# Optimization experiments

Measured on AMD Instinct MI355X. Metric: run time of the kernel, lower is better.

The kernel has to match this reference:

```python
import jax, jax.numpy as jnp
import numpy as np
import math

N_NODES = 100000
N_EDGES = 1600000
IN_FEATS = 128
H_FEATS = 64
NUM_CLASSES = 2
D = 2  # num_layers -> d+1 = 3 filters, each polynomial of degree d


def _calc_thetas(d):
    # Beta-Bernstein polynomial coefficients, ascending powers of x.
    # f_i(x) = (x/2)^i (1-x/2)^(d-i) / B(i+1, d+1-i),  B = i!(d-i)!/(d+1)!
    thetas = []
    for i in range(d + 1):
        beta = math.factorial(i) * math.factorial(d - i) / math.factorial(d + 1)
        p = np.array([1.0])
        for _ in range(i):
            p = np.convolve(p, [0.0, 0.5])
        for _ in range(d - i):
            p = np.convolve(p, [1.0, -0.5])
        thetas.append([float(c) for c in (p / beta)])
    return thetas

THETAS = _calc_thetas(D)


def setup_inputs() -> dict:
    key = jax.random.key(0)
    ks = jax.random.split(key, 12)
    x = jax.random.normal(ks[0], (N_NODES, IN_FEATS), dtype=jnp.float32)
    edge_index = jax.random.randint(ks[1], (2, N_EDGES), 0, N_NODES, dtype=jnp.int64)
    s = 0.05
    W1 = jax.random.normal(ks[2], (IN_FEATS, H_FEATS), jnp.float32) * s
    b1 = jnp.zeros((H_FEATS,), jnp.float32)
    W2 = jax.random.normal(ks[3], (H_FEATS, H_FEATS), jnp.float32) * s
    b2 = jnp.zeros((H_FEATS,), jnp.float32)
    Wm1 = jax.random.normal(ks[4], (H_FEATS * len(THETAS), H_FEATS), jnp.float32) * s
    bm1 = jnp.zeros((H_FEATS,), jnp.float32)
    Wm2 = jax.random.normal(ks[5], (H_FEATS, NUM_CLASSES), jnp.float32) * s
    bm2 = jnp.zeros((NUM_CLASSES,), jnp.float32)
    return {"x": x, "edge_index": edge_index, "W1": W1, "b1": b1,
            "W2": W2, "b2": b2, "Wm1": Wm1, "bm1": bm1, "Wm2": Wm2, "bm2": bm2}


def reference(x, edge_index, W1, b1, W2, b2, Wm1, bm1, Wm2, bm2):
    N = x.shape[0]
    src, dst = edge_index[0], edge_index[1]
    # in-degrees (edges point src -> dst, message summed at dst)
    deg = jax.ops.segment_sum(jnp.ones((edge_index.shape[1],), x.dtype), dst,
                              num_segments=N)
    dinv = jnp.clip(deg, 1.0, None) ** -0.5  # [N]
    dinv = dinv[:, None]
    # two linear + ReLU layers
    h = jax.nn.relu(x @ W1 + b1)
    h = jax.nn.relu(h @ W2 + b2)
    # PolyConv per theta: feat <- feat - D^-1/2 A D^-1/2 feat; acc += theta_k feat
    outs = []
    for theta in THETAS:
        feat = h
        acc = theta[0] * feat
        for k in range(1, len(theta)):
            msg = jax.ops.segment_sum((feat * dinv)[src], dst, num_segments=N)
            feat = feat - msg * dinv
            acc = acc + theta[k] * feat
        outs.append(acc)
    h_final = jnp.concatenate(outs, axis=-1)  # [N, h_feats*(d+1)]
    # MLP (2 layers): Linear -> ReLU -> Linear
    h_final = jax.nn.relu(h_final @ Wm1 + bm1)
    return h_final @ Wm2 + bm2
```

## Files before the change

### kernel.cpp

```cpp
#include <hip/hip_runtime.h>
#include <math.h>

#define N_NODES 100000
#define N_EDGES 1600000
#define IN_F 128
#define H_F 64

#define NBKT 196
#define BSEG 16384
#define BCAP 14336

#define NP        100096
#define OFF_CNT   0
#define OFF_MPK   256
#define OFF_W1H   6400
#define OFF_W1L   10496
#define OFF_W2H   14592
#define OFF_W2L   16640
#define OFF_OFFS  18688
#define OFF_D2    (OFF_OFFS + NP + 64)
#define OFF_RD    (OFF_D2 + NP)
#define OFF_DINV  (OFF_RD + NP)
#define OFF_ADJ   (OFF_DINV + NP)
#define OFF_H0    (OFF_ADJ + N_EDGES)
#define OFF_H1    (OFF_H0 + N_NODES*32)
#define OFF_H2    (OFF_H1 + N_NODES*32)

typedef __attribute__((ext_vector_type(8))) short bf16x8;
typedef __attribute__((ext_vector_type(4))) float f32x4;

__device__ __forceinline__ unsigned short bf16rn(float f) {
    unsigned u = __float_as_uint(f);
    u += 0x7FFFu + ((u >> 16) & 1u);
    return (unsigned short)(u >> 16);
}
#define UNPK(u, lo, hi) { lo = __uint_as_float((u) << 16); hi = __uint_as_float((u) & 0xFFFF0000u); }

__global__ __launch_bounds__(256) void k_prep(const float* __restrict__ Wm1,
        const float* __restrict__ W1, const float* __restrict__ W2,
        unsigned short* __restrict__ mpk,
        unsigned short* __restrict__ w1h, unsigned short* __restrict__ w1l,
        unsigned short* __restrict__ w2h, unsigned short* __restrict__ w2l) {
    int idx = blockIdx.x * 256 + threadIdx.x;
    if (idx < 12288) {
        int j = idx & 7;
        int n = (idx >> 3) & 63;
        int qd = (idx >> 9) & 3;
        int s = idx >> 11;
        int k = s * 32 + qd * 8 + j;
        int p = k >> 6;
        int kk = k & 63;
        float w0 = Wm1[kk * 64 + n];
        float w1 = Wm1[(64 + kk) * 64 + n];
        float w2 = Wm1[(128 + kk) * 64 + n];
        float v;
        if (p == 0)      v = 3.0f * w0;
        else if (p == 1) v = 3.0f * (w1 - w0);
        else             v = 0.75f * (w0 + w2) - 1.5f * w1;
        mpk[idx] = bf16rn(v);
    } else if (idx < 12288 + 8192) {
        int lin = idx - 12288;
        int j = lin & 7, cc = (lin >> 3) & 15, ot = (lin >> 7) & 3;
        int qd = (lin >> 9) & 3, ks = lin >> 11;
        float v = W1[(ks * 32 + qd * 8 + j) * 64 + ot * 16 + cc];
        unsigned short h = bf16rn(v);
        w1h[lin] = h;
        w1l[lin] = bf16rn(v - __uint_as_float((unsigned)h << 16));
    } else if (idx < 24576) {
        int lin = idx - 20480;
        int j = lin & 7, cc = (lin >> 3) & 15, ot = (lin >> 7) & 3;
        int qd = (lin >> 9) & 3, ks = lin >> 11;
        float v = W2[(ks * 32 + qd * 8 + j) * 64 + ot * 16 + cc];
        unsigned short h = bf16rn(v);
        w2h[lin] = h;
        w2l[lin] = bf16rn(v - __uint_as_float((unsigned)h << 16));
    }
}

__global__ __launch_bounds__(256) void k_bin(const int* __restrict__ src,
        const int* __restrict__ dst, int* __restrict__ cnt,
        int* __restrict__ binned, int E) {
    __shared__ int hist[4][208];
    __shared__ int cur4[4][208];
    int t = threadIdx.x;
    int w = t >> 6;
    for (int i = t; i < 4 * 208; i += 256) (&hist[0][0])[i] = 0;
    __syncthreads();
    int base = blockIdx.x * 4096 + t;
    int d[16];
    #pragma unroll
    for (int i = 0; i < 16; ++i) {
        int e = base + i * 256;
        int dd = (e < E) ? dst[e] : -1;
        d[i] = dd;
        if (dd >= 0) atomicAdd(&hist[w][dd >> 9], 1);
    }
    __syncthreads();
    if (t < NBKT) {
        int h0 = hist[0][t], h1 = hist[1][t], h2 = hist[2][t], h3 = hist[3][t];
        int tot = h0 + h1 + h2 + h3;
        int b0 = (tot > 0) ? atomicAdd(&cnt[t], tot) : 0;
        cur4[0][t] = b0;
        cur4[1][t] = b0 + h0;
        cur4[2][t] = b0 + h0 + h1;
        cur4[3][t] = b0 + h0 + h1 + h2;
    }
    __syncthreads();
    #pragma unroll
    for (int i = 0; i < 16; ++i) {
        int e = base + i * 256;
        if (e < E) {
            int s = src[e];
            int dd = d[i];
            int b = dd >> 9;
            int p = atomicAdd(&cur4[w][b], 1);
            if (p < BSEG) binned[b * BSEG + p] = ((dd & 511) << 17) | s;
        }
    }
}

__global__ __launch_bounds__(256) void k_cfill(const int* __restrict__ binned,
        const int* __restrict__ cnt, int* __restrict__ offs, int* __restrict__ adj,
        float* __restrict__ d2a, float* __restrict__ rda, float* __restrict__ dinva) {
    __shared__ int csum[256];
    __shared__ int degl[512];
    __shared__ int offl[512];
    __shared__ int curl[512];
    __shared__ int wsum[4];
    __shared__ int adjl[BCAP];
    int b = blockIdx.x, t = threadIdx.x;
    int cv = (t < NBKT) ? cnt[t] : 0;
    csum[t] = cv;
    __syncthreads();
    #pragma unroll
    for (int off = 1; off < 256; off <<= 1) {
        int u = (t >= off) ? csum[t - off] : 0;
        __syncthreads();
        csum[t] += u;
        __syncthreads();
    }
    int baseb = (b == 0) ? 0 : csum[b - 1];
    int cntb = csum[b] - baseb;
    if (b == 0 && t == 0) offs[N_NODES] = N_EDGES;
    int n0 = b << 9;
    const int* bp = binned + b * BSEG;
    degl[2 * t] = 0; degl[2 * t + 1] = 0;
    __syncthreads();
    for (int i = t; i < cntb; i += 256) {
        int w = bp[i];
        atomicAdd(&degl[w >> 17], 1);
    }
    __syncthreads();
    int d0 = degl[2 * t], d1 = degl[2 * t + 1];
    int tot = d0 + d1;
    int lane = t & 63, wid = t >> 6;
    int inc = tot;
    #pragma unroll
    for (int off = 1; off < 64; off <<= 1) {
        int v = __shfl_up(inc, off, 64);
        if (lane >= off) inc += v;
    }
    if (lane == 63) wsum[wid] = inc;
    __syncthreads();
    int wb = 0;
    for (int w = 0; w < wid; ++w) wb += wsum[w];
    int excl = wb + inc - tot;
    offl[2 * t] = excl;          curl[2 * t] = excl;
    offl[2 * t + 1] = excl + d0; curl[2 * t + 1] = excl + d0;
    __syncthreads();
    #pragma unroll
    for (int rep = 0; rep < 2; ++rep) {
        int i = t + rep * 256;
        int n = n0 + i;
        if (n < N_NODES) {
            offs[n] = baseb + offl[i];
            float df = (float)degl[i];
            if (df < 1.f) df = 1.f;
            float di = 1.0f / sqrtf(df);
            dinva[n] = di;
            d2a[n] = di * di;
            rda[n] = sqrtf(df);
        }
    }
    for (int i = t; i < cntb; i += 256) {
        int w = bp[i];
        int loc = w >> 17;
        int s = w & 0x1FFFF;
        int p = atomicAdd(&curl[loc], 1);
        if (p < BCAP) adjl[p] = s;
        else adj[baseb + p] = s;
    }
    __syncthreads();
    int lim = cntb < BCAP ? cntb : BCAP;
    for (int i = t; i < lim; i += 256) adj[baseb + i] = adjl[i];
}

__global__ __launch_bounds__(256) void k_gemm12(const float* __restrict__ x,
        const unsigned short* __restrict__ w1h, const unsigned short* __restrict__ w1l,
        const unsigned short* __restrict__ w2h, const unsigned short* __restrict__ w2l,
        const float* __restrict__ b1, const float* __restrict__ b2,
        const float* __restrict__ dinva, unsigned short* __restrict__ gsh, int N) {
    __shared__ unsigned int Hl[4][16 * 65];
    __shared__ unsigned short Sl[4][16 * 66];
    int t = threadIdx.x;
    int w = t >> 6, lane = t & 63;
    int c = lane & 15, qd = lane >> 4;
    int nbase = blockIdx.x * 64 + w * 16;
    if (nbase >= N) return;
    int node = nbase + c;
    int nclamp = (node < N) ? node : N - 1;

    f32x4 a0 = {0.f,0.f,0.f,0.f}, a1 = a0, a2 = a0, a3 = a0;
    #pragma unroll
    for (int ks = 0; ks < 4; ++ks) {
        const float* xp = x + (size_t)nclamp * IN_F + ks * 32 + qd * 8;
        float4 xa = *(const float4*)xp;
        float4 xb = *(const float4*)(xp + 4);
        float xs[8] = {xa.x, xa.y, xa.z, xa.w, xb.x, xb.y, xb.z, xb.w};
        bf16x8 ahi, alo;
        #pragma unroll
        for (int j = 0; j < 8; ++j) {
            unsigned short h = bf16rn(xs[j]);
            ahi[j] = (short)h;
            alo[j] = (short)bf16rn(xs[j] - __uint_as_float((unsigned)h << 16));
        }
        const unsigned short* bh = w1h + (size_t)(ks * 4 + qd) * 512;
        const unsigned short* bl = w1l + (size_t)(ks * 4 + qd) * 512;
        bf16x8 h0 = *(const bf16x8*)(bh + 0 * 128 + c * 8);
        bf16x8 l0 = *(const bf16x8*)(bl + 0 * 128 + c * 8);
        bf16x8 h1 = *(const bf16x8*)(bh + 1 * 128 + c * 8);
        bf16x8 l1 = *(const bf16x8*)(bl + 1 * 128 + c * 8);
        bf16x8 h2 = *(const bf16x8*)(bh + 2 * 128 + c * 8);
        bf16x8 l2 = *(const bf16x8*)(bl + 2 * 128 + c * 8);
        bf16x8 h3 = *(const bf16x8*)(bh + 3 * 128 + c * 8);
        bf16x8 l3 = *(const bf16x8*)(bl + 3 * 128 + c * 8);
        a0 = __builtin_amdgcn_mfma_f32_16x16x32_bf16(ahi, h0, a0, 0, 0, 0);
        a1 = __builtin_amdgcn_mfma_f32_16x16x32_bf16(ahi, h1, a1, 0, 0, 0);
        a2 = __builtin_amdgcn_mfma_f32_16x16x32_bf16(ahi, h2, a2, 0, 0, 0);
        a3 = __builtin_amdgcn_mfma_f32_16x16x32_bf16(ahi, h3, a3, 0, 0, 0);
        a0 = __builtin_amdgcn_mfma_f32_16x16x32_bf16(alo, h0, a0, 0, 0, 0);
        a1 = __builtin_amdgcn_mfma_f32_16x16x32_bf16(alo, h1, a1, 0, 0, 0);
        a2 = __builtin_amdgcn_mfma_f32_16x16x32_bf16(alo, h2, a2, 0, 0, 0);
        a3 = __builtin_amdgcn_mfma_f32_16x16x32_bf16(alo, h3, a3, 0, 0, 0);
        a0 = __builtin_amdgcn_mfma_f32_16x16x32_bf16(ahi, l0, a0, 0, 0, 0);
        a1 = __builtin_amdgcn_mfma_f32_16x16x32_bf16(ahi, l1, a1, 0, 0, 0);
        a2 = __builtin_amdgcn_mfma_f32_16x16x32_bf16(ahi, l2, a2, 0, 0, 0);
        a3 = __builtin_amdgcn_mfma_f32_16x16x32_bf16(ahi, l3, a3, 0, 0, 0);
    }
    #pragma unroll
    for (int ot = 0; ot < 4; ++ot) {
        float bb = b1[ot * 16 + c];
        f32x4 a = (ot == 0) ? a0 : (ot == 1) ? a1 : (ot == 2) ? a2 : a3;
        #pragma unroll
        for (int r = 0; r < 4; ++r) {
            float h = fmaxf(a[r] + bb, 0.f);
            unsigned short hh = bf16rn(h);
            unsigned short hl = bf16rn(h - __uint_as_float((unsigned)hh << 16));
            Hl[w][(qd * 4 + r) * 65 + ot * 16 + c] = ((unsigned)hh << 16) | hl;
        }
    }
    f32x4 d0 = {0.f,0.f,0.f,0.f}, d1 = d0, d2 = d0, d3 = d0;
    #pragma unroll
    for (int ks = 0; ks < 2; ++ks) {
        bf16x8 ahi, alo;
        #pragma unroll
        for (int j = 0; j < 8; ++j) {
            unsigned v = Hl[w][c * 65 + ks * 32 + qd * 8 + j];
            ahi[j] = (short)(v >> 16);
            alo[j] = (short)(v & 0xFFFFu);
        }
        const unsigned short* bh = w2h + (size_t)(ks * 4 + qd) * 512;
        const unsigned short* bl = w2l + (size_t)(ks * 4 + qd) * 512;
        bf16x8 h0 = *(const bf16x8*)(bh + 0 * 128 + c * 8);
        bf16x8 l0 = *(const bf16x8*)(bl + 0 * 128 + c * 8);
        bf16x8 h1 = *(const bf16x8*)(bh + 1 * 128 + c * 8);
        bf16x8 l1 = *(const bf16x8*)(bl + 1 * 128 + c * 8);
        bf16x8 h2 = *(const bf16x8*)(bh + 2 * 128 + c * 8);
        bf16x8 l2 = *(const bf16x8*)(bl + 2 * 128 + c * 8);
        bf16x8 h3 = *(const bf16x8*)(bh + 3 * 128 + c * 8);
        bf16x8 l3 = *(const bf16x8*)(bl + 3 * 128 + c * 8);
        d0 = __builtin_amdgcn_mfma_f32_16x16x32_bf16(ahi, h0, d0, 0, 0, 0);
        d1 = __builtin_amdgcn_mfma_f32_16x16x32_bf16(ahi, h1, d1, 0, 0, 0);
        d2 = __builtin_amdgcn_mfma_f32_16x16x32_bf16(ahi, h2, d2, 0, 0, 0);
        d3 = __builtin_amdgcn_mfma_f32_16x16x32_bf16(ahi, h3, d3, 0, 0, 0);
        d0 = __builtin_amdgcn_mfma_f32_16x16x32_bf16(alo, h0, d0, 0, 0, 0);
        d1 = __builtin_amdgcn_mfma_f32_16x16x32_bf16(alo, h1, d1, 0, 0, 0);
        d2 = __builtin_amdgcn_mfma_f32_16x16x32_bf16(alo, h2, d2, 0, 0, 0);
        d3 = __builtin_amdgcn_mfma_f32_16x16x32_bf16(alo, h3, d3, 0, 0, 0);
        d0 = __builtin_amdgcn_mfma_f32_16x16x32_bf16(ahi, l0, d0, 0, 0, 0);
        d1 = __builtin_amdgcn_mfma_f32_16x16x32_bf16(ahi, l1, d1, 0, 0, 0);
        d2 = __builtin_amdgcn_mfma_f32_16x16x32_bf16(ahi, l2, d2, 0, 0, 0);
        d3 = __builtin_amdgcn_mfma_f32_16x16x32_bf16(ahi, l3, d3, 0, 0, 0);
    }
    #pragma unroll
    for (int ot = 0; ot < 4; ++ot) {
        float bb = b2[ot * 16 + c];
        f32x4 a = (ot == 0) ? d0 : (ot == 1) ? d1 : (ot == 2) ? d2 : d3;
        #pragma unroll
        for (int r = 0; r < 4; ++r) {
            int nd = nbase + qd * 4 + r;
            float di = dinva[(nd < N) ? nd : N - 1];
            Sl[w][(qd * 4 + r) * 66 + ot * 16 + c] = bf16rn(di * fmaxf(a[r] + bb, 0.f));
        }
    }
    #pragma unroll
    for (int i = 0; i < 4; ++i) {
        int nl = i * 4 + qd;
        int nd = nbase + nl;
        if (nd < N) {
            ushort4 v;
            v.x = Sl[w][nl * 66 + c * 4 + 0];
            v.y = Sl[w][nl * 66 + c * 4 + 1];
            v.z = Sl[w][nl * 66 + c * 4 + 2];
            v.w = Sl[w][nl * 66 + c * 4 + 3];
            *(ushort4*)(gsh + (size_t)nd * 64 + c * 4) = v;
        }
    }
}

__global__ __launch_bounds__(256) void k_prop(const unsigned short* __restrict__ gh,
        unsigned short* __restrict__ gout, const int* __restrict__ offs,
        const int* __restrict__ adj, const float* __restrict__ d2a, int N) {
    int t = threadIdx.x;
    int lane = t & 63;
    int g = lane >> 3;
    int q = lane & 7;
    int n = blockIdx.x * 4 + (t >> 6);
    if (n >= N) return;
    int beg = offs[n], end = offs[n + 1];
    float a0 = 0.f, a1 = 0.f, a2 = 0.f, a3 = 0.f;
    float a4 = 0.f, a5 = 0.f, a6 = 0.f, a7 = 0.f;
    int e = beg + g;
    for (; e + 24 < end; e += 32) {
        int s0 = adj[e], s1 = adj[e + 8], s2 = adj[e + 16], s3 = adj[e + 24];
        uint4 v0 = *(const uint4*)(gh + (size_t)s0 * 64 + 8 * q);
        uint4 v1 = *(const uint4*)(gh + (size_t)s1 * 64 + 8 * q);
        uint4 v2 = *(const uint4*)(gh + (size_t)s2 * 64 + 8 * q);
        uint4 v3 = *(const uint4*)(gh + (size_t)s3 * 64 + 8 * q);
        float l, h;
        UNPK(v0.x, l, h); a0 += l; a1 += h;
        UNPK(v0.y, l, h); a2 += l; a3 += h;
        UNPK(v0.z, l, h); a4 += l; a5 += h;
        UNPK(v0.w, l, h); a6 += l; a7 += h;
        UNPK(v1.x, l, h); a0 += l; a1 += h;
        UNPK(v1.y, l, h); a2 += l; a3 += h;
        UNPK(v1.z, l, h); a4 += l; a5 += h;
        UNPK(v1.w, l, h); a6 += l; a7 += h;
        UNPK(v2.x, l, h); a0 += l; a1 += h;
        UNPK(v2.y, l, h); a2 += l; a3 += h;
        UNPK(v2.z, l, h); a4 += l; a5 += h;
        UNPK(v2.w, l, h); a6 += l; a7 += h;
        UNPK(v3.x, l, h); a0 += l; a1 += h;
        UNPK(v3.y, l, h); a2 += l; a3 += h;
        UNPK(v3.z, l, h); a4 += l; a5 += h;
        UNPK(v3.w, l, h); a6 += l; a7 += h;
    }
    for (; e < end; e += 8) {
        int s = adj[e];
        uint4 v = *(const uint4*)(gh + (size_t)s * 64 + 8 * q);
        float l, h;
        UNPK(v.x, l, h); a0 += l; a1 += h;
        UNPK(v.y, l, h); a2 += l; a3 += h;
        UNPK(v.z, l, h); a4 += l; a5 += h;
        UNPK(v.w, l, h); a6 += l; a7 += h;
    }
    #pragma unroll
    for (int m = 8; m < 64; m <<= 1) {
        a0 += __shfl_xor(a0, m); a1 += __shfl_xor(a1, m);
        a2 += __shfl_xor(a2, m); a3 += __shfl_xor(a3, m);
        a4 += __shfl_xor(a4, m); a5 += __shfl_xor(a5, m);
        a6 += __shfl_xor(a6, m); a7 += __shfl_xor(a7, m);
    }
    if (g == 0) {
        float d2n = d2a[n];
        uint4 sv = *(const uint4*)(gh + (size_t)n * 64 + 8 * q);
        float l, h;
        uint4 r;
        UNPK(sv.x, l, h);
        r.x = ((unsigned)bf16rn(fmaf(-d2n, a1, h)) << 16) | bf16rn(fmaf(-d2n, a0, l));
        UNPK(sv.y, l, h);
        r.y = ((unsigned)bf16rn(fmaf(-d2n, a3, h)) << 16) | bf16rn(fmaf(-d2n, a2, l));
        UNPK(sv.z, l, h);
        r.z = ((unsigned)bf16rn(fmaf(-d2n, a5, h)) << 16) | bf16rn(fmaf(-d2n, a4, l));
        UNPK(sv.w, l, h);
        r.w = ((unsigned)bf16rn(fmaf(-d2n, a7, h)) << 16) | bf16rn(fmaf(-d2n, a6, l));
        *(uint4*)(gout + (size_t)n * 64 + 8 * q) = r;
    }
}

__global__ __launch_bounds__(256) void k_final(const unsigned short* __restrict__ g0h,
        const unsigned short* __restrict__ g1h, const unsigned short* __restrict__ g2h,
        const unsigned short* __restrict__ mpk, const float* __restrict__ bm1,
        const float* __restrict__ Wm2, const float* __restrict__ bm2,
        const float* __restrict__ rda, float* __restrict__ out, int N) {
    int t = threadIdx.x;
    int w = t >> 6, lane = t & 63;
    int c = lane & 15, qd = lane >> 4;
    int nbase = blockIdx.x * 64 + w * 16;
    if (nbase >= N) return;
    int node = nbase + c;
    int nclamp = (node < N) ? node : N - 1;
    const unsigned short* bufs[3] = {g0h, g1h, g2h};
    f32x4 acc0 = {0.f, 0.f, 0.f, 0.f};
    f32x4 acc1 = {0.f, 0.f, 0.f, 0.f};
    f32x4 acc2 = {0.f, 0.f, 0.f, 0.f};
    f32x4 acc3 = {0.f, 0.f, 0.f, 0.f};
    #pragma unroll
    for (int s = 0; s < 6; ++s) {
        const unsigned short* gp = bufs[s >> 1];
        int k0 = (s & 1) * 32;
        bf16x8 a = *(const bf16x8*)(gp + (size_t)nclamp * 64 + k0 + qd * 8);
        const unsigned short* mb = mpk + (size_t)((s * 4 + qd) * 64) * 8;
        bf16x8 b0 = *(const bf16x8*)(mb + (size_t)(c) * 8);
        bf16x8 b1 = *(const bf16x8*)(mb + (size_t)(16 + c) * 8);
        bf16x8 b2 = *(const bf16x8*)(mb + (size_t)(32 + c) * 8);
        bf16x8 b3 = *(const bf16x8*)(mb + (size_t)(48 + c) * 8);
        acc0 = __builtin_amdgcn_mfma_f32_16x16x32_bf16(a, b0, acc0, 0, 0, 0);
        acc1 = __builtin_amdgcn_mfma_f32_16x16x32_bf16(a, b1, acc1, 0, 0, 0);
        acc2 = __builtin_amdgcn_mfma_f32_16x16x32_bf16(a, b2, acc2, 0, 0, 0);
        acc3 = __builtin_amdgcn_mfma_f32_16x16x32_bf16(a, b3, acc3, 0, 0, 0);
    }
    float rdr[4];
    #pragma unroll
    for (int r = 0; r < 4; ++r) {
        int nd = nbase + qd * 4 + r;
        rdr[r] = rda[(nd < N) ? nd : N - 1];
    }
    float p0[4] = {0.f, 0.f, 0.f, 0.f};
    float p1[4] = {0.f, 0.f, 0.f, 0.f};
    #pragma unroll
    for (int ot = 0; ot < 4; ++ot) {
        int col = ot * 16 + c;
        float bmc = bm1[col];
        float wc0 = Wm2[col * 2 + 0];
        float wc1 = Wm2[col * 2 + 1];
        f32x4 a = (ot == 0) ? acc0 : (ot == 1) ? acc1 : (ot == 2) ? acc2 : acc3;
        #pragma unroll
        for (int r = 0; r < 4; ++r) {
            float h = fmaxf(fmaf(rdr[r], a[r], bmc), 0.f);
            p0[r] = fmaf(h, wc0, p0[r]);
            p1[r] = fmaf(h, wc1, p1[r]);
        }
    }
    #pragma unroll
    for (int m = 1; m < 16; m <<= 1) {
        #pragma unroll
        for (int r = 0; r < 4; ++r) {
            p0[r] += __shfl_xor(p0[r], m);
            p1[r] += __shfl_xor(p1[r], m);
        }
    }
    if (c == 0) {
        float bo0 = bm2[0], bo1 = bm2[1];
        #pragma unroll
        for (int r = 0; r < 4; ++r) {
            int nd = nbase + qd * 4 + r;
            if (nd < N) {
                float2 o;
                o.x = p0[r] + bo0;
                o.y = p1[r] + bo1;
                *(float2*)(out + (size_t)nd * 2) = o;
            }
        }
    }
}

extern "C" void kernel_launch(void* const* d_in, const int* in_sizes, int n_in,
                              void* d_out, int out_size, void* d_ws, size_t ws_size,
                              hipStream_t stream) {
    const float* x   = (const float*)d_in[0];
    const int*   ei  = (const int*)d_in[1];
    const float* W1  = (const float*)d_in[2];
    const float* b1  = (const float*)d_in[3];
    const float* W2  = (const float*)d_in[4];
    const float* b2  = (const float*)d_in[5];
    const float* Wm1 = (const float*)d_in[6];
    const float* bm1 = (const float*)d_in[7];
    const float* Wm2 = (const float*)d_in[8];
    const float* bm2 = (const float*)d_in[9];
    float* out = (float*)d_out;

    int* ws = (int*)d_ws;
    int*   cnt   = ws + OFF_CNT;
    unsigned short* mpk = (unsigned short*)(ws + OFF_MPK);
    unsigned short* w1h = (unsigned short*)(ws + OFF_W1H);
    unsigned short* w1l = (unsigned short*)(ws + OFF_W1L);
    unsigned short* w2h = (unsigned short*)(ws + OFF_W2H);
    unsigned short* w2l = (unsigned short*)(ws + OFF_W2L);
    int*   offs  = ws + OFF_OFFS;
    float* d2a   = (float*)(ws + OFF_D2);
    float* rda   = (float*)(ws + OFF_RD);
    float* dinva = (float*)(ws + OFF_DINV);
    int*   adj   = ws + OFF_ADJ;
    unsigned short* gs0h = (unsigned short*)(ws + OFF_H0);
    unsigned short* gs1h = (unsigned short*)(ws + OFF_H1);
    unsigned short* gs2h = (unsigned short*)(ws + OFF_H2);
    int*   binned = ws + OFF_H1;

    const int* srcp = ei;
    const int* dstp = ei + N_EDGES;

    hipMemsetAsync(cnt, 0, 256 * sizeof(int), stream);

    k_prep<<<96, 256, 0, stream>>>(Wm1, W1, W2, mpk, w1h, w1l, w2h, w2l);
    k_bin<<<(N_EDGES + 4095) / 4096, 256, 0, stream>>>(srcp, dstp, cnt, binned, N_EDGES);
    k_cfill<<<NBKT, 256, 0, stream>>>(binned, cnt, offs, adj, d2a, rda, dinva);

    int nblk = (N_NODES + 63) / 64;
    k_gemm12<<<nblk, 256, 0, stream>>>(x, w1h, w1l, w2h, w2l, b1, b2, dinva, gs0h, N_NODES);

    k_prop<<<(N_NODES + 3) / 4, 256, 0, stream>>>(gs0h, gs1h, offs, adj, d2a, N_NODES);
    k_prop<<<(N_NODES + 3) / 4, 256, 0, stream>>>(gs1h, gs2h, offs, adj, d2a, N_NODES);

    k_final<<<nblk, 256, 0, stream>>>(gs0h, gs1h, gs2h, mpk, bm1, Wm2, bm2, rda, out, N_NODES);
}
```

Before: 270.1 us.

## Use finer destination buckets for CSR build and software-pipeline propagation gathers

Halves the destination bucket width from 512 to 256 nodes, doubling the number of buckets and cfill blocks, and shrinks per-bucket shared staging so more blocks can run at once. The bucket-count zeroing moves from a memset into the prep kernel, and k_bin processes half as many edges per block. The propagation kernel swaps its 4-way unrolled gather for a one-ahead prefetch loop and loads the self row and degree scale before the edge loop. Smaller bucket capacity raises the chance of overflow for skewed degree distributions, and the simpler prop loop keeps fewer loads in flight.

```diff
diff --git a/kernel.cpp b/kernel.cpp
--- a/kernel.cpp
+++ b/kernel.cpp
@@ -6,18 +6,18 @@
 #define IN_F 128
 #define H_F 64
 
-#define NBKT 196
-#define BSEG 16384
-#define BCAP 14336
+#define NBKT 391
+#define BSEG 5120
+#define BCAP 5120
 
 #define NP        100096
 #define OFF_CNT   0
-#define OFF_MPK   256
-#define OFF_W1H   6400
-#define OFF_W1L   10496
-#define OFF_W2H   14592
-#define OFF_W2L   16640
-#define OFF_OFFS  18688
+#define OFF_MPK   512
+#define OFF_W1H   6656
+#define OFF_W1L   10752
+#define OFF_W2H   14848
+#define OFF_W2L   16896
+#define OFF_OFFS  18944
 #define OFF_D2    (OFF_OFFS + NP + 64)
 #define OFF_RD    (OFF_D2 + NP)
 #define OFF_DINV  (OFF_RD + NP)
@@ -40,8 +40,10 @@
         const float* __restrict__ W1, const float* __restrict__ W2,
         unsigned short* __restrict__ mpk,
         unsigned short* __restrict__ w1h, unsigned short* __restrict__ w1l,
-        unsigned short* __restrict__ w2h, unsigned short* __restrict__ w2l) {
+        unsigned short* __restrict__ w2h, unsigned short* __restrict__ w2l,
+        int* __restrict__ cnt) {
     int idx = blockIdx.x * 256 + threadIdx.x;
+    if (idx < 512) cnt[idx] = 0;
     if (idx < 12288) {
         int j = idx & 7;
         int n = (idx >> 3) & 63;
@@ -80,41 +82,41 @@
 __global__ __launch_bounds__(256) void k_bin(const int* __restrict__ src,
         const int* __restrict__ dst, int* __restrict__ cnt,
         int* __restrict__ binned, int E) {
-    __shared__ int hist[4][208];
-    __shared__ int cur4[4][208];
+    __shared__ int hist[4][NBKT + 1];
+    __shared__ int cur4[4][NBKT + 1];
     int t = threadIdx.x;
     int w = t >> 6;
-    for (int i = t; i < 4 * 208; i += 256) (&hist[0][0])[i] = 0;
-    __syncthreads();
-    int base = blockIdx.x * 4096 + t;
-    int d[16];
-    #pragma unroll
-    for (int i = 0; i < 16; ++i) {
+    for (int i = t; i < 4 * (NBKT + 1); i += 256) (&hist[0][0])[i] = 0;
+    __syncthreads();
+    int base = blockIdx.x * 2048 + t;
+    int d[8];
+    #pragma unroll
+    for (int i = 0; i < 8; ++i) {
         int e = base + i * 256;
         int dd = (e < E) ? dst[e] : -1;
         d[i] = dd;
-        if (dd >= 0) atomicAdd(&hist[w][dd >> 9], 1);
-    }
-    __syncthreads();
-    if (t < NBKT) {
-        int h0 = hist[0][t], h1 = hist[1][t], h2 = hist[2][t], h3 = hist[3][t];
+        if (dd >= 0) atomicAdd(&hist[w][dd >> 8], 1);
+    }
+    __syncthreads();
+    for (int i = t; i < NBKT; i += 256) {
+        int h0 = hist[0][i], h1 = hist[1][i], h2 = hist[2][i], h3 = hist[3][i];
         int tot = h0 + h1 + h2 + h3;
-        int b0 = (tot > 0) ? atomicAdd(&cnt[t], tot) : 0;
-        cur4[0][t] = b0;
-        cur4[1][t] = b0 + h0;
-        cur4[2][t] = b0 + h0 + h1;
-        cur4[3][t] = b0 + h0 + h1 + h2;
-    }
-    __syncthreads();
-    #pragma unroll
-    for (int i = 0; i < 16; ++i) {
+        int b0 = (tot > 0) ? atomicAdd(&cnt[i], tot) : 0;
+        cur4[0][i] = b0;
+        cur4[1][i] = b0 + h0;
+        cur4[2][i] = b0 + h0 + h1;
+        cur4[3][i] = b0 + h0 + h1 + h2;
+    }
+    __syncthreads();
+    #pragma unroll
+    for (int i = 0; i < 8; ++i) {
         int e = base + i * 256;
         if (e < E) {
             int s = src[e];
             int dd = d[i];
-            int b = dd >> 9;
+            int b = dd >> 8;
             int p = atomicAdd(&cur4[w][b], 1);
-            if (p < BSEG) binned[b * BSEG + p] = ((dd & 511) << 17) | s;
+            if (p < BSEG) binned[b * BSEG + p] = ((dd & 255) << 17) | s;
         }
     }
 }
@@ -123,14 +125,15 @@
         const int* __restrict__ cnt, int* __restrict__ offs, int* __restrict__ adj,
         float* __restrict__ d2a, float* __restrict__ rda, float* __restrict__ dinva) {
     __shared__ int csum[256];
-    __shared__ int degl[512];
-    __shared__ int offl[512];
-    __shared__ int curl[512];
+    __shared__ int degl[256];
+    __shared__ int curl[256];
     __shared__ int wsum[4];
     __shared__ int adjl[BCAP];
     int b = blockIdx.x, t = threadIdx.x;
-    int cv = (t < NBKT) ? cnt[t] : 0;
-    csum[t] = cv;
+    int p = 0;
+    if (2 * t < NBKT) p += cnt[2 * t];
+    if (2 * t + 1 < NBKT) p += cnt[2 * t + 1];
+    csum[t] = p;
     __syncthreads();
     #pragma unroll
     for (int off = 1; off < 256; off <<= 1) {
@@ -139,22 +142,19 @@
         csum[t] += u;
         __syncthreads();
     }
-    int baseb = (b == 0) ? 0 : csum[b - 1];
-    int cntb = csum[b] - baseb;
+    int b2 = b >> 1;
+    int baseb = ((b2 > 0) ? csum[b2 - 1] : 0) + ((b & 1) ? cnt[b - 1] : 0);
+    int cntb = cnt[b];
     if (b == 0 && t == 0) offs[N_NODES] = N_EDGES;
-    int n0 = b << 9;
+    int n0 = b << 8;
     const int* bp = binned + b * BSEG;
-    degl[2 * t] = 0; degl[2 * t + 1] = 0;
-    __syncthreads();
-    for (int i = t; i < cntb; i += 256) {
-        int w = bp[i];
-        atomicAdd(&degl[w >> 17], 1);
-    }
-    __syncthreads();
-    int d0 = degl[2 * t], d1 = degl[2 * t + 1];
-    int tot = d0 + d1;
+    degl[t] = 0;
+    __syncthreads();
+    for (int i = t; i < cntb; i += 256) atomicAdd(&degl[bp[i] >> 17], 1);
+    __syncthreads();
+    int d0 = degl[t];
     int lane = t & 63, wid = t >> 6;
-    int inc = tot;
+    int inc = d0;
     #pragma unroll
     for (int off = 1; off < 64; off <<= 1) {
         int v = __shfl_up(inc, off, 64);
@@ -164,31 +164,26 @@
     __syncthreads();
     int wb = 0;
     for (int w = 0; w < wid; ++w) wb += wsum[w];
-    int excl = wb + inc - tot;
-    offl[2 * t] = excl;          curl[2 * t] = excl;
-    offl[2 * t + 1] = excl + d0; curl[2 * t + 1] = excl + d0;
-    __syncthreads();
-    #pragma unroll
-    for (int rep = 0; rep < 2; ++rep) {
-        int i = t + rep * 256;
-        int n = n0 + i;
-        if (n < N_NODES) {
-            offs[n] = baseb + offl[i];
-            float df = (float)degl[i];
-            if (df < 1.f) df = 1.f;
-            float di = 1.0f / sqrtf(df);
-            dinva[n] = di;
-            d2a[n] = di * di;
-            rda[n] = sqrtf(df);
-        }
-    }
+    int excl = wb + inc - d0;
+    curl[t] = excl;
+    int n = n0 + t;
+    if (n < N_NODES) {
+        offs[n] = baseb + excl;
+        float df = (float)d0;
+        if (df < 1.f) df = 1.f;
+        float di = 1.0f / sqrtf(df);
+        dinva[n] = di;
+        d2a[n] = di * di;
+        rda[n] = sqrtf(df);
+    }
+    __syncthreads();
     for (int i = t; i < cntb; i += 256) {
         int w = bp[i];
         int loc = w >> 17;
         int s = w & 0x1FFFF;
-        int p = atomicAdd(&curl[loc], 1);
-        if (p < BCAP) adjl[p] = s;
-        else adj[baseb + p] = s;
+        int pp = atomicAdd(&curl[loc], 1);
+        if (pp < BCAP) adjl[pp] = s;
+        else adj[baseb + pp] = s;
     }
     __syncthreads();
     int lim = cntb < BCAP ? cntb : BCAP;
@@ -328,36 +323,24 @@
     int n = blockIdx.x * 4 + (t >> 6);
     if (n >= N) return;
     int beg = offs[n], end = offs[n + 1];
+    float d2n = d2a[n];
+    uint4 sv = *(const uint4*)(gh + (size_t)n * 64 + 8 * q);
     float a0 = 0.f, a1 = 0.f, a2 = 0.f, a3 = 0.f;
     float a4 = 0.f, a5 = 0.f, a6 = 0.f, a7 = 0.f;
     int e = beg + g;
-    for (; e + 24 < end; e += 32) {
-        int s0 = adj[e], s1 = adj[e + 8], s2 = adj[e + 16], s3 = adj[e + 24];
-        uint4 v0 = *(const uint4*)(gh + (size_t)s0 * 64 + 8 * q);
-        uint4 v1 = *(const uint4*)(gh + (size_t)s1 * 64 + 8 * q);
-        uint4 v2 = *(const uint4*)(gh + (size_t)s2 * 64 + 8 * q);
-        uint4 v3 = *(const uint4*)(gh + (size_t)s3 * 64 + 8 * q);
-        float l, h;
-        UNPK(v0.x, l, h); a0 += l; a1 += h;
-        UNPK(v0.y, l, h); a2 += l; a3 += h;
-        UNPK(v0.z, l, h); a4 += l; a5 += h;
-        UNPK(v0.w, l, h); a6 += l; a7 += h;
-        UNPK(v1.x, l, h); a0 += l; a1 += h;
-        UNPK(v1.y, l, h); a2 += l; a3 += h;
-        UNPK(v1.z, l, h); a4 += l; a5 += h;
-        UNPK(v1.w, l, h); a6 += l; a7 += h;
-        UNPK(v2.x, l, h); a0 += l; a1 += h;
-        UNPK(v2.y, l, h); a2 += l; a3 += h;
-        UNPK(v2.z, l, h); a4 += l; a5 += h;
-        UNPK(v2.w, l, h); a6 += l; a7 += h;
-        UNPK(v3.x, l, h); a0 += l; a1 += h;
-        UNPK(v3.y, l, h); a2 += l; a3 += h;
-        UNPK(v3.z, l, h); a4 += l; a5 += h;
-        UNPK(v3.w, l, h); a6 += l; a7 += h;
-    }
-    for (; e < end; e += 8) {
+    if (e < end) {
         int s = adj[e];
         uint4 v = *(const uint4*)(gh + (size_t)s * 64 + 8 * q);
+        for (e += 8; e < end; e += 8) {
+            int s2 = adj[e];
+            uint4 v2 = *(const uint4*)(gh + (size_t)s2 * 64 + 8 * q);
+            float l, h;
+            UNPK(v.x, l, h); a0 += l; a1 += h;
+            UNPK(v.y, l, h); a2 += l; a3 += h;
+            UNPK(v.z, l, h); a4 += l; a5 += h;
+            UNPK(v.w, l, h); a6 += l; a7 += h;
+            v = v2;
+        }
         float l, h;
         UNPK(v.x, l, h); a0 += l; a1 += h;
         UNPK(v.y, l, h); a2 += l; a3 += h;
@@ -372,8 +355,6 @@
         a6 += __shfl_xor(a6, m); a7 += __shfl_xor(a7, m);
     }
     if (g == 0) {
-        float d2n = d2a[n];
-        uint4 sv = *(const uint4*)(gh + (size_t)n * 64 + 8 * q);
         float l, h;
         uint4 r;
         UNPK(sv.x, l, h);
@@ -500,10 +481,8 @@
     const int* srcp = ei;
     const int* dstp = ei + N_EDGES;
 
-    hipMemsetAsync(cnt, 0, 256 * sizeof(int), stream);
-
-    k_prep<<<96, 256, 0, stream>>>(Wm1, W1, W2, mpk, w1h, w1l, w2h, w2l);
-    k_bin<<<(N_EDGES + 4095) / 4096, 256, 0, stream>>>(srcp, dstp, cnt, binned, N_EDGES);
+    k_prep<<<96, 256, 0, stream>>>(Wm1, W1, W2, mpk, w1h, w1l, w2h, w2l, cnt);
+    k_bin<<<(N_EDGES + 2047) / 2048, 256, 0, stream>>>(srcp, dstp, cnt, binned, N_EDGES);
     k_cfill<<<NBKT, 256, 0, stream>>>(binned, cnt, offs, adj, d2a, rda, dinva);
 
     int nblk = (N_NODES + 63) / 64;
```

Measured after the change: 254.2 us. -5.9%, faster.
